# Kernel tuning notes

Measured on AMD Instinct MI355X. Metric: run time of the kernel, lower is better.

Reference implementation:

```python
import jax, jax.numpy as jnp
import numpy as np

EPS = 1e-5
NEG_SLOPE = 0.1


def setup_inputs() -> dict:
    key = jax.random.key(0)
    ks = jax.random.split(key, 4)
    B, Cin, Cout, D, E, EMB = 2, 32, 32, 40, 3, 1
    return {
        "x": jax.random.normal(ks[0], (B, Cin, D, D, D), dtype=jnp.float32),
        "embedding": jax.random.normal(ks[1], (B, EMB), dtype=jnp.float32),
        "route_w": jax.random.normal(ks[2], (EMB, E), dtype=jnp.float32),
        "route_b": jnp.zeros((E,), dtype=jnp.float32),
        "expert_kernels": jax.random.normal(ks[3], (E, Cout, Cin, 3, 3, 3), dtype=jnp.float32) * 0.05,
        "expert_bias": jnp.zeros((E, Cout), dtype=jnp.float32),
        "gamma": jnp.ones((Cout,), dtype=jnp.float32),
        "beta": jnp.zeros((Cout,), dtype=jnp.float32),
    }


def reference(x, embedding, route_w, route_b, expert_kernels, expert_bias, gamma, beta):
    # CondConv routing: sigmoid(Linear(embedding)) -> per-sample expert weights [B, E]
    r = jax.nn.sigmoid(embedding @ route_w + route_b)
    # Per-sample combined kernel [B, O, I, 3, 3, 3] and bias [B, O]
    w = jnp.einsum('be,eoixyz->boixyz', r, expert_kernels)
    b = r @ expert_bias

    def conv_one(xi, wi):
        # xi: [Cin, D, H, W], wi: [O, I, 3, 3, 3] -> [Cout, D, H, W]
        return jax.lax.conv_general_dilated(
            xi[None], wi, window_strides=(1, 1, 1), padding='SAME',
            dimension_numbers=('NCDHW', 'OIDHW', 'NCDHW'))[0]

    y = jax.vmap(conv_one)(x, w) + b[:, :, None, None, None]  # [B, O, D, H, W]

    # BatchNorm3d (training mode: biased batch stats over B,D,H,W per channel)
    mean = jnp.mean(y, axis=(0, 2, 3, 4), keepdims=True)
    var = jnp.mean(jnp.square(y - mean), axis=(0, 2, 3, 4), keepdims=True)
    y = (y - mean) * jax.lax.rsqrt(var + EPS)
    y = y * gamma[None, :, None, None, None] + beta[None, :, None, None, None]

    # LeakyReLU(0.1)
    y = jnp.where(y >= 0, y, NEG_SLOPE * y)

    # Upsample nearest, scale_factor=2 on all 3 spatial dims
    y = jnp.repeat(jnp.repeat(jnp.repeat(y, 2, axis=2), 2, axis=3), 2, axis=4)
    return y
```

## Files before the change

kernel.cpp:

```cpp
#include <hip/hip_runtime.h>
#include <hip/hip_bf16.h>
#include <math.h>

#define BB   2
#define CIN  32
#define COUT 32
#define DM   40
#define PD   42
#define NPTS (DM*DM)
#define NVOL (DM*DM*DM)
#define EPSBN 1e-5f
#define NSLOT 64

typedef short  bf16x8  __attribute__((ext_vector_type(8)));
typedef short  bf16x4  __attribute__((ext_vector_type(4)));
typedef float  floatx4 __attribute__((ext_vector_type(4)));

#define WS_WFRAG 0
#define WS_BCOMB 27648
#define WS_SUM2  27712
#define WS_XPAD2 31808
#define WS_Y     2402624

#define REPACK_BLOCKS (PD*PD*BB)
#define NW_ELEMS  (2*2*27*64*8)
#define PREP_ELEMS (NW_ELEMS + 64 + NSLOT*64)
#define PREP_BLOCKS ((PREP_ELEMS + 255) / 256)

static __device__ __forceinline__ short f2bf(float f) {
    __hip_bfloat16 h = __float2bfloat16(f);
    return *reinterpret_cast<short*>(&h);
}
static __device__ __forceinline__ float bf2f(short s) {
    union { unsigned u; float f; } cv;
    cv.u = ((unsigned)(unsigned short)s) << 16;
    return cv.f;
}

__global__ void prep_repack_kernel(const float* __restrict__ x,
                                   const float* __restrict__ emb,
                                   const float* __restrict__ rw,
                                   const float* __restrict__ rb,
                                   const float* __restrict__ ek,
                                   const float* __restrict__ ebias,
                                   float* __restrict__ ws) {
    __shared__ __hip_bfloat16 tile[PD * 32];
    const int bid = blockIdx.x;
    const int t = threadIdx.x;
    if (bid < REPACK_BLOCKS) {
        int b  = bid / (PD * PD);
        int r  = bid % (PD * PD);
        int zp = r / PD, yp = r % PD;
        __hip_bfloat16* row = (__hip_bfloat16*)(ws + WS_XPAD2) +
                              ((((size_t)b * PD + zp) * PD + yp) * PD) * 32;
        const bool inz = (zp >= 1 && zp <= DM && yp >= 1 && yp <= DM);
        const int i  = t >> 3;
        const int xl = t & 7;
        #pragma unroll
        for (int k = 0; k < 6; ++k) {
            int xp = xl + 8 * k;
            if (xp < PD) {
                float v = 0.0f;
                if (inz && xp >= 1 && xp <= DM)
                    v = x[(size_t)(b * CIN + i) * NVOL +
                          (zp - 1) * NPTS + (yp - 1) * DM + (xp - 1)];
                tile[xp * 32 + i] = __float2bfloat16(v);
            }
        }
        __syncthreads();
        const unsigned* ts = (const unsigned*)tile;
        unsigned* rowu = (unsigned*)row;
        for (int j = t; j < PD * 32 / 2; j += 256) rowu[j] = ts[j];
        return;
    }
    int idx = (bid - REPACK_BLOCKS) * 256 + t;
    __hip_bfloat16* wfrag = (__hip_bfloat16*)(ws + WS_WFRAG);
    if (idx < NW_ELEMS) {
        int j    = idx & 7;
        int lane = (idx >> 3) & 63;
        int tap  = (idx >> 9) % 27;
        int nt   = (idx / (27 * 512)) & 1;
        int b    = idx / (2 * 27 * 512);
        int o = nt * 16 + (lane & 15);
        int i = (lane >> 4) * 8 + j;
        float e0 = emb[b];
        float w = 0.0f;
        #pragma unroll
        for (int e = 0; e < 3; ++e) {
            float r = 1.0f / (1.0f + expf(-(e0 * rw[e] + rb[e])));
            w += r * ek[((e * COUT + o) * CIN + i) * 27 + tap];
        }
        wfrag[idx] = __float2bfloat16(w);
    } else if (idx < NW_ELEMS + 64) {
        int j2 = idx - NW_ELEMS;
        int b = j2 >> 5, o = j2 & 31;
        float e0 = emb[b];
        float bv = 0.0f;
        #pragma unroll
        for (int e = 0; e < 3; ++e) {
            float r = 1.0f / (1.0f + expf(-(e0 * rw[e] + rb[e])));
            bv += r * ebias[e * COUT + o];
        }
        ws[WS_BCOMB + j2] = bv;
    } else if (idx < PREP_ELEMS) {
        ws[WS_SUM2 + (idx - NW_ELEMS - 64)] = 0.0f;
    }
}

__global__ __launch_bounds__(256, 4) void conv_mfma_kernel(
        const __hip_bfloat16* __restrict__ xp2,
        const bf16x8* __restrict__ wfrag,
        const float* __restrict__ bcomb,
        __hip_bfloat16* __restrict__ y,
        float* __restrict__ sums2) {
    const int mc = blockIdx.x, z = blockIdx.y, b = blockIdx.z;
    const int tid = threadIdx.x, lane = tid & 63, wv = tid >> 6;
    const int mt = wv & 1, nt = wv >> 1;
    const int quad = lane >> 4, l15 = lane & 15;

    __shared__ float lstat[64];
    __shared__ short ytile[32 * 72];

    if (tid < 64) lstat[tid] = 0.0f;
    __syncthreads();

    const int pa0 = mc * 64 + mt * 32 + l15;
    const int pa1 = pa0 + 16;
    const int ya0 = pa0 / DM, xa0 = pa0 % DM;
    const int ya1 = pa1 / DM, xa1 = pa1 % DM;
    const char* abase0 = (const char*)xp2 +
        ((((size_t)b * PD + z) * PD + ya0) * PD + xa0) * 64 + quad * 16;
    const char* abase1 = (const char*)xp2 +
        ((((size_t)b * PD + z) * PD + ya1) * PD + xa1) * 64 + quad * 16;
    const bf16x8* wbase = wfrag + ((b * 2 + nt) * 27) * 64 + lane;

    floatx4 acc0 = {0.f, 0.f, 0.f, 0.f};
    floatx4 acc1 = {0.f, 0.f, 0.f, 0.f};
    #pragma unroll
    for (int t = 0; t < 27; ++t) {
        const int dz = t / 9, dy = (t / 3) % 3, dx = t % 3;
        const int aoff = ((dz * PD + dy) * PD + dx) * 64;
        bf16x8 av0 = *(const bf16x8*)(abase0 + aoff);
        bf16x8 av1 = *(const bf16x8*)(abase1 + aoff);
        bf16x8 bv  = wbase[t * 64];
        acc0 = __builtin_amdgcn_mfma_f32_16x16x32_bf16(av0, bv, acc0, 0, 0, 0);
        acc1 = __builtin_amdgcn_mfma_f32_16x16x32_bf16(av1, bv, acc1, 0, 0, 0);
    }

    const int o = nt * 16 + l15;
    const float bias = bcomb[b * COUT + o];

    float u0 = acc0[0] + bias, u1 = acc0[1] + bias;
    float u2 = acc0[2] + bias, u3 = acc0[3] + bias;
    float w0 = acc1[0] + bias, w1 = acc1[1] + bias;
    float w2 = acc1[2] + bias, w3 = acc1[3] + bias;

    {
        const int s0 = mt * 32 + quad * 4;
        bf16x4 p0 = { f2bf(u0), f2bf(u1), f2bf(u2), f2bf(u3) };
        bf16x4 p1 = { f2bf(w0), f2bf(w1), f2bf(w2), f2bf(w3) };
        *(bf16x4*)&ytile[o * 72 + s0]      = p0;
        *(bf16x4*)&ytile[o * 72 + s0 + 16] = p1;
    }

    float vs = u0 + u1 + u2 + u3 + w0 + w1 + w2 + w3;
    float vq = u0*u0 + u1*u1 + u2*u2 + u3*u3 + w0*w0 + w1*w1 + w2*w2 + w3*w3;
    vs += __shfl_xor(vs, 16); vq += __shfl_xor(vq, 16);
    vs += __shfl_xor(vs, 32); vq += __shfl_xor(vq, 32);
    if (lane < 16) {
        atomicAdd(&lstat[o],      vs);
        atomicAdd(&lstat[32 + o], vq);
    }
    __syncthreads();

    {
        const int o2 = tid >> 3, c = tid & 7;
        bf16x8 v = *(const bf16x8*)&ytile[o2 * 72 + c * 8];
        __hip_bfloat16* dst = y + ((size_t)(b * COUT + o2) * DM + z) * NPTS
                            + mc * 64 + c * 8;
        *(bf16x8*)dst = v;
    }
    if (tid < 64) {
        int slot = ((b * DM + z) * 25 + mc) & (NSLOT - 1);
        atomicAdd(&sums2[slot * 64 + tid], lstat[tid]);
    }
}

__global__ __launch_bounds__(256) void upsample_kernel(
        const __hip_bfloat16* __restrict__ yin,
        const float* __restrict__ sums2,
        const float* __restrict__ gamma,
        const float* __restrict__ beta,
        float* __restrict__ out) {
    __shared__ float partl[4][64];
    __shared__ float ssc[32], ssh[32];
    __shared__ float fplane[NPTS];
    const int tid = threadIdx.x;
    const int cc  = blockIdx.x / DM;
    const int z   = blockIdx.x % DM;
    const int c   = cc & 31;

    {
        int sg = tid >> 6, st = tid & 63;
        float p = 0.0f;
        #pragma unroll
        for (int s = 0; s < 16; ++s) p += sums2[(sg * 16 + s) * 64 + st];
        partl[sg][st] = p;
    }
    __syncthreads();
    if (tid < 64) {
        partl[0][tid] += partl[1][tid] + partl[2][tid] + partl[3][tid];
    }
    __syncthreads();
    if (tid < 32) {
        const float invN = 1.0f / (float)(BB * NVOL);
        float mean  = partl[0][tid] * invN;
        float var   = partl[0][32 + tid] * invN - mean * mean;
        float scale = gamma[tid] * rsqrtf(var + EPSBN);
        ssc[tid] = scale;
        ssh[tid] = beta[tid] - mean * scale;
    }
    __syncthreads();

    const float sc = ssc[c], sh = ssh[c];
    if (tid < NPTS / 8) {
        bf16x8 rv = *(const bf16x8*)(yin + ((size_t)cc * DM + z) * NPTS + tid * 8);
        #pragma unroll
        for (int j = 0; j < 8; ++j) {
            float v = bf2f(rv[j]) * sc + sh;
            fplane[tid * 8 + j] = (v >= 0.0f) ? v : 0.1f * v;
        }
    }
    __syncthreads();

    float* outp = out + ((size_t)cc * 80 + 2 * z) * 6400;
    #pragma unroll 2
    for (int cch = tid; cch < 2 * 1600; cch += 256) {
        int plane = cch >> 10 >= 0 ? (cch / 1600) : 0;
        int cp    = cch - plane * 1600;
        int yy2   = cp / 20;
        int sx0   = (cp % 20) * 2;
        const float* srow = fplane + (yy2 >> 1) * DM;
        float v0 = srow[sx0], v1 = srow[sx0 + 1];
        floatx4 q = {v0, v0, v1, v1};
        *(floatx4*)(outp + (size_t)plane * 6400 + cp * 4) = q;
    }
}

extern "C" void kernel_launch(void* const* d_in, const int* in_sizes, int n_in,
                              void* d_out, int out_size, void* d_ws, size_t ws_size,
                              hipStream_t stream) {
    const float* x     = (const float*)d_in[0];
    const float* emb   = (const float*)d_in[1];
    const float* rw    = (const float*)d_in[2];
    const float* rb    = (const float*)d_in[3];
    const float* ek    = (const float*)d_in[4];
    const float* ebias = (const float*)d_in[5];
    const float* gamma = (const float*)d_in[6];
    const float* beta  = (const float*)d_in[7];
    float* ws  = (float*)d_ws;
    float* out = (float*)d_out;

    prep_repack_kernel<<<REPACK_BLOCKS + PREP_BLOCKS, 256, 0, stream>>>(
        x, emb, rw, rb, ek, ebias, ws);

    conv_mfma_kernel<<<dim3(25, DM, BB), 256, 0, stream>>>(
        (const __hip_bfloat16*)(ws + WS_XPAD2), (const bf16x8*)(ws + WS_WFRAG),
        ws + WS_BCOMB, (__hip_bfloat16*)(ws + WS_Y), ws + WS_SUM2);

    upsample_kernel<<<BB * COUT * DM, 256, 0, stream>>>(
        (const __hip_bfloat16*)(ws + WS_Y), ws + WS_SUM2, gamma, beta, out);
}
```

Baseline: 197.6 us.

## Fuse prep, conv and upsample into one persistent kernel with grid barriers

```diff
diff --git a/kernel.cpp b/kernel.cpp
--- a/kernel.cpp
+++ b/kernel.cpp
@@ -12,6 +12,8 @@
 #define EPSBN 1e-5f
 #define NSLOT 64
 
+#define GRID 1000
+
 typedef short  bf16x8  __attribute__((ext_vector_type(8)));
 typedef short  bf16x4  __attribute__((ext_vector_type(4)));
 typedef float  floatx4 __attribute__((ext_vector_type(4)));
@@ -21,11 +23,14 @@
 #define WS_SUM2  27712
 #define WS_XPAD2 31808
 #define WS_Y     2402624
+#define WS_BAR   4450624
 
 #define REPACK_BLOCKS (PD*PD*BB)
 #define NW_ELEMS  (2*2*27*64*8)
 #define PREP_ELEMS (NW_ELEMS + 64 + NSLOT*64)
-#define PREP_BLOCKS ((PREP_ELEMS + 255) / 256)
+#define PREP_UNITS (REPACK_BLOCKS + (PREP_ELEMS + 255) / 256)
+#define CONV_UNITS (25 * DM * BB)
+#define UP_UNITS   (BB * COUT * DM)
 
 static __device__ __forceinline__ short f2bf(float f) {
     __hip_bfloat16 h = __float2bfloat16(f);
@@ -37,213 +42,256 @@
     return cv.f;
 }
 
-__global__ void prep_repack_kernel(const float* __restrict__ x,
-                                   const float* __restrict__ emb,
-                                   const float* __restrict__ rw,
-                                   const float* __restrict__ rb,
-                                   const float* __restrict__ ek,
-                                   const float* __restrict__ ebias,
-                                   float* __restrict__ ws) {
-    __shared__ __hip_bfloat16 tile[PD * 32];
-    const int bid = blockIdx.x;
-    const int t = threadIdx.x;
-    if (bid < REPACK_BLOCKS) {
-        int b  = bid / (PD * PD);
-        int r  = bid % (PD * PD);
-        int zp = r / PD, yp = r % PD;
-        __hip_bfloat16* row = (__hip_bfloat16*)(ws + WS_XPAD2) +
-                              ((((size_t)b * PD + zp) * PD + yp) * PD) * 32;
-        const bool inz = (zp >= 1 && zp <= DM && yp >= 1 && yp <= DM);
-        const int i  = t >> 3;
-        const int xl = t & 7;
-        #pragma unroll
-        for (int k = 0; k < 6; ++k) {
-            int xp = xl + 8 * k;
-            if (xp < PD) {
-                float v = 0.0f;
-                if (inz && xp >= 1 && xp <= DM)
-                    v = x[(size_t)(b * CIN + i) * NVOL +
-                          (zp - 1) * NPTS + (yp - 1) * DM + (xp - 1)];
-                tile[xp * 32 + i] = __float2bfloat16(v);
-            }
-        }
-        __syncthreads();
-        const unsigned* ts = (const unsigned*)tile;
-        unsigned* rowu = (unsigned*)row;
-        for (int j = t; j < PD * 32 / 2; j += 256) rowu[j] = ts[j];
-        return;
-    }
-    int idx = (bid - REPACK_BLOCKS) * 256 + t;
-    __hip_bfloat16* wfrag = (__hip_bfloat16*)(ws + WS_WFRAG);
-    if (idx < NW_ELEMS) {
-        int j    = idx & 7;
-        int lane = (idx >> 3) & 63;
-        int tap  = (idx >> 9) % 27;
-        int nt   = (idx / (27 * 512)) & 1;
-        int b    = idx / (2 * 27 * 512);
-        int o = nt * 16 + (lane & 15);
-        int i = (lane >> 4) * 8 + j;
-        float e0 = emb[b];
-        float w = 0.0f;
-        #pragma unroll
-        for (int e = 0; e < 3; ++e) {
-            float r = 1.0f / (1.0f + expf(-(e0 * rw[e] + rb[e])));
-            w += r * ek[((e * COUT + o) * CIN + i) * 27 + tap];
-        }
-        wfrag[idx] = __float2bfloat16(w);
-    } else if (idx < NW_ELEMS + 64) {
-        int j2 = idx - NW_ELEMS;
-        int b = j2 >> 5, o = j2 & 31;
-        float e0 = emb[b];
-        float bv = 0.0f;
-        #pragma unroll
-        for (int e = 0; e < 3; ++e) {
-            float r = 1.0f / (1.0f + expf(-(e0 * rw[e] + rb[e])));
-            bv += r * ebias[e * COUT + o];
-        }
-        ws[WS_BCOMB + j2] = bv;
-    } else if (idx < PREP_ELEMS) {
-        ws[WS_SUM2 + (idx - NW_ELEMS - 64)] = 0.0f;
-    }
-}
-
-__global__ __launch_bounds__(256, 4) void conv_mfma_kernel(
-        const __hip_bfloat16* __restrict__ xp2,
-        const bf16x8* __restrict__ wfrag,
-        const float* __restrict__ bcomb,
-        __hip_bfloat16* __restrict__ y,
-        float* __restrict__ sums2) {
-    const int mc = blockIdx.x, z = blockIdx.y, b = blockIdx.z;
-    const int tid = threadIdx.x, lane = tid & 63, wv = tid >> 6;
-    const int mt = wv & 1, nt = wv >> 1;
-    const int quad = lane >> 4, l15 = lane & 15;
-
-    __shared__ float lstat[64];
-    __shared__ short ytile[32 * 72];
-
-    if (tid < 64) lstat[tid] = 0.0f;
+static __device__ __forceinline__ void grid_barrier_once(unsigned* cnt,
+                                                         unsigned* flag) {
     __syncthreads();
-
-    const int pa0 = mc * 64 + mt * 32 + l15;
-    const int pa1 = pa0 + 16;
-    const int ya0 = pa0 / DM, xa0 = pa0 % DM;
-    const int ya1 = pa1 / DM, xa1 = pa1 % DM;
-    const char* abase0 = (const char*)xp2 +
-        ((((size_t)b * PD + z) * PD + ya0) * PD + xa0) * 64 + quad * 16;
-    const char* abase1 = (const char*)xp2 +
-        ((((size_t)b * PD + z) * PD + ya1) * PD + xa1) * 64 + quad * 16;
-    const bf16x8* wbase = wfrag + ((b * 2 + nt) * 27) * 64 + lane;
-
-    floatx4 acc0 = {0.f, 0.f, 0.f, 0.f};
-    floatx4 acc1 = {0.f, 0.f, 0.f, 0.f};
-    #pragma unroll
-    for (int t = 0; t < 27; ++t) {
-        const int dz = t / 9, dy = (t / 3) % 3, dx = t % 3;
-        const int aoff = ((dz * PD + dy) * PD + dx) * 64;
-        bf16x8 av0 = *(const bf16x8*)(abase0 + aoff);
-        bf16x8 av1 = *(const bf16x8*)(abase1 + aoff);
-        bf16x8 bv  = wbase[t * 64];
-        acc0 = __builtin_amdgcn_mfma_f32_16x16x32_bf16(av0, bv, acc0, 0, 0, 0);
-        acc1 = __builtin_amdgcn_mfma_f32_16x16x32_bf16(av1, bv, acc1, 0, 0, 0);
-    }
-
-    const int o = nt * 16 + l15;
-    const float bias = bcomb[b * COUT + o];
-
-    float u0 = acc0[0] + bias, u1 = acc0[1] + bias;
-    float u2 = acc0[2] + bias, u3 = acc0[3] + bias;
-    float w0 = acc1[0] + bias, w1 = acc1[1] + bias;
-    float w2 = acc1[2] + bias, w3 = acc1[3] + bias;
-
-    {
-        const int s0 = mt * 32 + quad * 4;
-        bf16x4 p0 = { f2bf(u0), f2bf(u1), f2bf(u2), f2bf(u3) };
-        bf16x4 p1 = { f2bf(w0), f2bf(w1), f2bf(w2), f2bf(w3) };
-        *(bf16x4*)&ytile[o * 72 + s0]      = p0;
-        *(bf16x4*)&ytile[o * 72 + s0 + 16] = p1;
-    }
-
-    float vs = u0 + u1 + u2 + u3 + w0 + w1 + w2 + w3;
-    float vq = u0*u0 + u1*u1 + u2*u2 + u3*u3 + w0*w0 + w1*w1 + w2*w2 + w3*w3;
-    vs += __shfl_xor(vs, 16); vq += __shfl_xor(vq, 16);
-    vs += __shfl_xor(vs, 32); vq += __shfl_xor(vq, 32);
-    if (lane < 16) {
-        atomicAdd(&lstat[o],      vs);
-        atomicAdd(&lstat[32 + o], vq);
+    if (threadIdx.x == 0) {
+        __threadfence();
+        if (atomicAdd(cnt, 1u) == (unsigned)(GRID - 1)) {
+            __hip_atomic_store(flag, 1u, __ATOMIC_RELEASE,
+                               __HIP_MEMORY_SCOPE_AGENT);
+        } else {
+            int spins = 0;
+            while (!__hip_atomic_load(flag, __ATOMIC_ACQUIRE,
+                                      __HIP_MEMORY_SCOPE_AGENT)) {
+                __builtin_amdgcn_s_sleep(4);
+                if (++spins > (1 << 22)) break;
+            }
+        }
+        __threadfence();
     }
     __syncthreads();
-
-    {
-        const int o2 = tid >> 3, c = tid & 7;
-        bf16x8 v = *(const bf16x8*)&ytile[o2 * 72 + c * 8];
-        __hip_bfloat16* dst = y + ((size_t)(b * COUT + o2) * DM + z) * NPTS
-                            + mc * 64 + c * 8;
-        *(bf16x8*)dst = v;
-    }
-    if (tid < 64) {
-        int slot = ((b * DM + z) * 25 + mc) & (NSLOT - 1);
-        atomicAdd(&sums2[slot * 64 + tid], lstat[tid]);
-    }
-}
-
-__global__ __launch_bounds__(256) void upsample_kernel(
-        const __hip_bfloat16* __restrict__ yin,
-        const float* __restrict__ sums2,
+}
+
+__global__ __launch_bounds__(256, 4) void fused_kernel(
+        const float* __restrict__ x,
+        const float* __restrict__ emb,
+        const float* __restrict__ rw,
+        const float* __restrict__ rb,
+        const float* __restrict__ ek,
+        const float* __restrict__ ebias,
         const float* __restrict__ gamma,
         const float* __restrict__ beta,
+        float* __restrict__ ws,
         float* __restrict__ out) {
-    __shared__ float partl[4][64];
-    __shared__ float ssc[32], ssh[32];
-    __shared__ float fplane[NPTS];
-    const int tid = threadIdx.x;
-    const int cc  = blockIdx.x / DM;
-    const int z   = blockIdx.x % DM;
-    const int c   = cc & 31;
+    const int bid = blockIdx.x;
+    const int t   = threadIdx.x;
+    unsigned* bar = (unsigned*)(ws + WS_BAR);
+
+    __shared__ union {
+        short ptile[PD * 32];
+        struct { float lstat[64]; short ytile[32 * 72]; } c;
+        struct { float partl[4][64]; float ssc[32]; float ssh[32];
+                 float fplane[NPTS]; } up;
+    } sm;
+
+    for (int u = bid; u < PREP_UNITS; u += GRID) {
+        if (u < REPACK_BLOCKS) {
+            int b  = u / (PD * PD);
+            int r  = u % (PD * PD);
+            int zp = r / PD, yp = r % PD;
+            short* row = (short*)(ws + WS_XPAD2) +
+                         ((((size_t)b * PD + zp) * PD + yp) * PD) * 32;
+            const bool inz = (zp >= 1 && zp <= DM && yp >= 1 && yp <= DM);
+            const int i  = t >> 3;
+            const int xl = t & 7;
+            #pragma unroll
+            for (int k = 0; k < 6; ++k) {
+                int xp = xl + 8 * k;
+                if (xp < PD) {
+                    float v = 0.0f;
+                    if (inz && xp >= 1 && xp <= DM)
+                        v = x[(size_t)(b * CIN + i) * NVOL +
+                              (zp - 1) * NPTS + (yp - 1) * DM + (xp - 1)];
+                    sm.ptile[xp * 32 + i] = f2bf(v);
+                }
+            }
+            __syncthreads();
+            const unsigned* ts = (const unsigned*)sm.ptile;
+            unsigned* rowu = (unsigned*)row;
+            for (int j = t; j < PD * 32 / 2; j += 256) rowu[j] = ts[j];
+        } else {
+            int idx = (u - REPACK_BLOCKS) * 256 + t;
+            short* wfrag = (short*)(ws + WS_WFRAG);
+            if (idx < NW_ELEMS) {
+                int j    = idx & 7;
+                int lane = (idx >> 3) & 63;
+                int tap  = (idx >> 9) % 27;
+                int nt   = (idx / (27 * 512)) & 1;
+                int b    = idx / (2 * 27 * 512);
+                int o = nt * 16 + (lane & 15);
+                int i = (lane >> 4) * 8 + j;
+                float e0 = emb[b];
+                float w = 0.0f;
+                #pragma unroll
+                for (int e = 0; e < 3; ++e) {
+                    float r = 1.0f / (1.0f + expf(-(e0 * rw[e] + rb[e])));
+                    w += r * ek[((e * COUT + o) * CIN + i) * 27 + tap];
+                }
+                wfrag[idx] = f2bf(w);
+            } else if (idx < NW_ELEMS + 64) {
+                int j2 = idx - NW_ELEMS;
+                int b = j2 >> 5, o = j2 & 31;
+                float e0 = emb[b];
+                float bv = 0.0f;
+                #pragma unroll
+                for (int e = 0; e < 3; ++e) {
+                    float r = 1.0f / (1.0f + expf(-(e0 * rw[e] + rb[e])));
+                    bv += r * ebias[e * COUT + o];
+                }
+                ws[WS_BCOMB + j2] = bv;
+            } else if (idx < PREP_ELEMS) {
+                ws[WS_SUM2 + (idx - NW_ELEMS - 64)] = 0.0f;
+            }
+        }
+        __syncthreads();
+    }
+
+    grid_barrier_once(&bar[0], &bar[1]);
 
     {
-        int sg = tid >> 6, st = tid & 63;
-        float p = 0.0f;
-        #pragma unroll
-        for (int s = 0; s < 16; ++s) p += sums2[(sg * 16 + s) * 64 + st];
-        partl[sg][st] = p;
+        const __hip_bfloat16* xp2 = (const __hip_bfloat16*)(ws + WS_XPAD2);
+        const bf16x8* wfrag = (const bf16x8*)(ws + WS_WFRAG);
+        const float* bcomb = ws + WS_BCOMB;
+        __hip_bfloat16* y = (__hip_bfloat16*)(ws + WS_Y);
+        float* sums2 = ws + WS_SUM2;
+
+        const int lane = t & 63, wv = t >> 6;
+        const int mt = wv & 1, nt = wv >> 1;
+        const int quad = lane >> 4, l15 = lane & 15;
+
+        for (int u = bid; u < CONV_UNITS; u += GRID) {
+            const int mc = u % 25;
+            const int z  = (u / 25) % DM;
+            const int b  = u / (25 * DM);
+
+            if (t < 64) sm.c.lstat[t] = 0.0f;
+            __syncthreads();
+
+            const int pa0 = mc * 64 + mt * 32 + l15;
+            const int pa1 = pa0 + 16;
+            const int ya0 = pa0 / DM, xa0 = pa0 % DM;
+            const int ya1 = pa1 / DM, xa1 = pa1 % DM;
+            const char* abase0 = (const char*)xp2 +
+                ((((size_t)b * PD + z) * PD + ya0) * PD + xa0) * 64 + quad * 16;
+            const char* abase1 = (const char*)xp2 +
+                ((((size_t)b * PD + z) * PD + ya1) * PD + xa1) * 64 + quad * 16;
+            const bf16x8* wbase = wfrag + ((b * 2 + nt) * 27) * 64 + lane;
+
+            floatx4 acc0 = {0.f, 0.f, 0.f, 0.f};
+            floatx4 acc1 = {0.f, 0.f, 0.f, 0.f};
+            #pragma unroll
+            for (int tap = 0; tap < 27; ++tap) {
+                const int dz = tap / 9, dy = (tap / 3) % 3, dx = tap % 3;
+                const int aoff = ((dz * PD + dy) * PD + dx) * 64;
+                bf16x8 av0 = *(const bf16x8*)(abase0 + aoff);
+                bf16x8 av1 = *(const bf16x8*)(abase1 + aoff);
+                bf16x8 bv  = wbase[tap * 64];
+                acc0 = __builtin_amdgcn_mfma_f32_16x16x32_bf16(av0, bv, acc0, 0, 0, 0);
+                acc1 = __builtin_amdgcn_mfma_f32_16x16x32_bf16(av1, bv, acc1, 0, 0, 0);
+            }
+
+            const int o = nt * 16 + l15;
+            const float bias = bcomb[b * COUT + o];
+
+            float u0 = acc0[0] + bias, u1 = acc0[1] + bias;
+            float u2 = acc0[2] + bias, u3 = acc0[3] + bias;
+            float w0 = acc1[0] + bias, w1 = acc1[1] + bias;
+            float w2 = acc1[2] + bias, w3 = acc1[3] + bias;
+
+            {
+                const int s0 = mt * 32 + quad * 4;
+                bf16x4 p0 = { f2bf(u0), f2bf(u1), f2bf(u2), f2bf(u3) };
+                bf16x4 p1 = { f2bf(w0), f2bf(w1), f2bf(w2), f2bf(w3) };
+                *(bf16x4*)&sm.c.ytile[o * 72 + s0]      = p0;
+                *(bf16x4*)&sm.c.ytile[o * 72 + s0 + 16] = p1;
+            }
+
+            float vs = u0 + u1 + u2 + u3 + w0 + w1 + w2 + w3;
+            float vq = u0*u0 + u1*u1 + u2*u2 + u3*u3
+                     + w0*w0 + w1*w1 + w2*w2 + w3*w3;
+            vs += __shfl_xor(vs, 16); vq += __shfl_xor(vq, 16);
+            vs += __shfl_xor(vs, 32); vq += __shfl_xor(vq, 32);
+            if (lane < 16) {
+                atomicAdd(&sm.c.lstat[o],      vs);
+                atomicAdd(&sm.c.lstat[32 + o], vq);
+            }
+            __syncthreads();
+
+            {
+                const int o2 = t >> 3, c = t & 7;
+                bf16x8 v = *(const bf16x8*)&sm.c.ytile[o2 * 72 + c * 8];
+                __hip_bfloat16* dst = y +
+                    ((size_t)(b * COUT + o2) * DM + z) * NPTS + mc * 64 + c * 8;
+                *(bf16x8*)dst = v;
+            }
+            if (t < 64) {
+                int slot = ((b * DM + z) * 25 + mc) & (NSLOT - 1);
+                atomicAdd(&sums2[slot * 64 + t], sm.c.lstat[t]);
+            }
+            __syncthreads();
+        }
     }
-    __syncthreads();
-    if (tid < 64) {
-        partl[0][tid] += partl[1][tid] + partl[2][tid] + partl[3][tid];
-    }
-    __syncthreads();
-    if (tid < 32) {
-        const float invN = 1.0f / (float)(BB * NVOL);
-        float mean  = partl[0][tid] * invN;
-        float var   = partl[0][32 + tid] * invN - mean * mean;
-        float scale = gamma[tid] * rsqrtf(var + EPSBN);
-        ssc[tid] = scale;
-        ssh[tid] = beta[tid] - mean * scale;
-    }
-    __syncthreads();
-
-    const float sc = ssc[c], sh = ssh[c];
-    if (tid < NPTS / 8) {
-        bf16x8 rv = *(const bf16x8*)(yin + ((size_t)cc * DM + z) * NPTS + tid * 8);
-        #pragma unroll
-        for (int j = 0; j < 8; ++j) {
-            float v = bf2f(rv[j]) * sc + sh;
-            fplane[tid * 8 + j] = (v >= 0.0f) ? v : 0.1f * v;
-        }
-    }
-    __syncthreads();
-
-    float* outp = out + ((size_t)cc * 80 + 2 * z) * 6400;
-    #pragma unroll 2
-    for (int cch = tid; cch < 2 * 1600; cch += 256) {
-        int plane = cch >> 10 >= 0 ? (cch / 1600) : 0;
-        int cp    = cch - plane * 1600;
-        int yy2   = cp / 20;
-        int sx0   = (cp % 20) * 2;
-        const float* srow = fplane + (yy2 >> 1) * DM;
-        float v0 = srow[sx0], v1 = srow[sx0 + 1];
-        floatx4 q = {v0, v0, v1, v1};
-        *(floatx4*)(outp + (size_t)plane * 6400 + cp * 4) = q;
+
+    grid_barrier_once(&bar[2], &bar[3]);
+
+    {
+        const __hip_bfloat16* yin = (const __hip_bfloat16*)(ws + WS_Y);
+        const float* sums2 = ws + WS_SUM2;
+
+        {
+            int sg = t >> 6, st = t & 63;
+            float p = 0.0f;
+            #pragma unroll
+            for (int s = 0; s < 16; ++s) p += sums2[(sg * 16 + s) * 64 + st];
+            sm.up.partl[sg][st] = p;
+        }
+        __syncthreads();
+        if (t < 64) {
+            sm.up.partl[0][t] += sm.up.partl[1][t] + sm.up.partl[2][t]
+                               + sm.up.partl[3][t];
+        }
+        __syncthreads();
+        if (t < 32) {
+            const float invN = 1.0f / (float)(BB * NVOL);
+            float mean  = sm.up.partl[0][t] * invN;
+            float var   = sm.up.partl[0][32 + t] * invN - mean * mean;
+            float scale = gamma[t] * rsqrtf(var + EPSBN);
+            sm.up.ssc[t] = scale;
+            sm.up.ssh[t] = beta[t] - mean * scale;
+        }
+        __syncthreads();
+
+        for (int u = bid; u < UP_UNITS; u += GRID) {
+            const int cc = u / DM;
+            const int z  = u % DM;
+            const int c  = cc & 31;
+            const float sc = sm.up.ssc[c], sh = sm.up.ssh[c];
+
+            if (t < NPTS / 8) {
+                bf16x8 rv = *(const bf16x8*)(yin +
+                    ((size_t)cc * DM + z) * NPTS + t * 8);
+                #pragma unroll
+                for (int j = 0; j < 8; ++j) {
+                    float v = bf2f(rv[j]) * sc + sh;
+                    sm.up.fplane[t * 8 + j] = (v >= 0.0f) ? v : 0.1f * v;
+                }
+            }
+            __syncthreads();
+
+            float* outp = out + ((size_t)cc * 80 + 2 * z) * 6400;
+            for (int cch = t; cch < 2 * 1600; cch += 256) {
+                int plane = cch / 1600;
+                int cp    = cch - plane * 1600;
+                int yy2   = cp / 20;
+                int sx0   = (cp % 20) * 2;
+                const float* srow = sm.up.fplane + (yy2 >> 1) * DM;
+                float v0 = srow[sx0], v1 = srow[sx0 + 1];
+                floatx4 q = {v0, v0, v1, v1};
+                *(floatx4*)(outp + (size_t)plane * 6400 + cp * 4) = q;
+            }
+            __syncthreads();
+        }
     }
 }
 
@@ -261,13 +309,8 @@
     float* ws  = (float*)d_ws;
     float* out = (float*)d_out;
 
-    prep_repack_kernel<<<REPACK_BLOCKS + PREP_BLOCKS, 256, 0, stream>>>(
-        x, emb, rw, rb, ek, ebias, ws);
-
-    conv_mfma_kernel<<<dim3(25, DM, BB), 256, 0, stream>>>(
-        (const __hip_bfloat16*)(ws + WS_XPAD2), (const bf16x8*)(ws + WS_WFRAG),
-        ws + WS_BCOMB, (__hip_bfloat16*)(ws + WS_Y), ws + WS_SUM2);
-
-    upsample_kernel<<<BB * COUT * DM, 256, 0, stream>>>(
-        (const __hip_bfloat16*)(ws + WS_Y), ws + WS_SUM2, gamma, beta, out);
-}
+    hipMemsetAsync(ws + WS_BAR, 0, 4 * sizeof(unsigned), stream);
+
+    fused_kernel<<<GRID, 256, 0, stream>>>(
+        x, emb, rw, rb, ek, ebias, gamma, beta, ws, out);
+}
```

New measurement: 553.0 us. +179.9%, slower.
